# Kernel tuning notes

Measured on AMD Instinct MI355X. Metric: run time of the kernel, lower is better.

## Reference

```python
import jax, jax.numpy as jnp
import numpy as np

HID = 128
N_LAYERS = 4


def setup_inputs() -> dict:
    key = jax.random.key(0)
    ks = jax.random.split(key, 16)
    B, T, N, F = 64, 168, 64, 17
    x = jax.random.normal(ks[0], (B, T, N, F), dtype=jnp.float32)
    adj = jax.random.randint(ks[1], (N, N), 0, 2, dtype=jnp.int32)
    s = 0.05
    W1 = jax.random.normal(ks[2], (F, HID), dtype=jnp.float32) * s
    a1 = jax.random.normal(ks[3], (2 * HID,), dtype=jnp.float32) * s
    W2 = jax.random.normal(ks[4], (HID, HID), dtype=jnp.float32) * s
    a2 = jax.random.normal(ks[5], (2 * HID,), dtype=jnp.float32) * s
    # PyTorch LSTM weights, 4 layers, gate order i,f,g,o; layer0 input=HID
    Wih = jax.random.normal(ks[6], (N_LAYERS, 4 * HID, HID), dtype=jnp.float32) * s
    Whh = jax.random.normal(ks[7], (N_LAYERS, 4 * HID, HID), dtype=jnp.float32) * s
    bih = jax.random.normal(ks[8], (N_LAYERS, 4 * HID), dtype=jnp.float32) * s
    bhh = jax.random.normal(ks[9], (N_LAYERS, 4 * HID), dtype=jnp.float32) * s
    Wlin = jax.random.normal(ks[10], (1, N_LAYERS * HID), dtype=jnp.float32) * s
    blin = jax.random.normal(ks[11], (1,), dtype=jnp.float32) * s
    return {"x": x, "adj": adj, "W1": W1, "a1": a1, "W2": W2, "a2": a2,
            "Wih": Wih, "Whh": Whh, "bih": bih, "bhh": bhh,
            "Wlin": Wlin, "blin": blin, "site_idx": 10}


def _gat(x, W, a, adj_mask):
    # x: [B,T,N,F] -> h: [B,T,N,O]; dense adjacency-masked attention
    h = jnp.einsum('btnf,fo->btno', x, W)
    O = W.shape[1]
    src = h @ a[:O]          # [B,T,N]  a^T[Wh_i || .]
    dst = h @ a[O:]          # [B,T,N]  a^T[. || Wh_j]
    e = jax.nn.leaky_relu(src[..., :, None] + dst[..., None, :], 0.2)  # [B,T,N,N]
    e = jnp.where(adj_mask, e, jnp.float32(-1e9))
    attn = jax.nn.softmax(e, axis=-1)
    return jnp.einsum('btij,btjo->btio', attn, h)


def _lstm_layer(x_seq, Wih_l, Whh_l, b_l):
    # x_seq: [B,T,H]; PyTorch gate order i,f,g,o
    B = x_seq.shape[0]
    h0 = jnp.zeros((B, HID), x_seq.dtype)

    def step(carry, x_t):
        h, c = carry
        g = x_t @ Wih_l.T + h @ Whh_l.T + b_l
        i, f, gg, o = jnp.split(g, 4, axis=-1)
        c = jax.nn.sigmoid(f) * c + jax.nn.sigmoid(i) * jnp.tanh(gg)
        h = jax.nn.sigmoid(o) * jnp.tanh(c)
        return (h, c), h

    (hT, cT), ys = jax.lax.scan(step, (h0, h0), jnp.swapaxes(x_seq, 0, 1))
    return jnp.swapaxes(ys, 0, 1), hT


def reference(x, adj, W1, a1, W2, a2, Wih, Whh, bih, bhh, Wlin, blin, site_idx):
    N = adj.shape[0]
    adj_mask = (adj > 0) | jnp.eye(N, dtype=bool)  # self-loops avoid empty rows
    h = _gat(x, W1, a1, adj_mask)
    h = _gat(h, W2, a2, adj_mask)
    seq = h[:, :, site_idx, :]                     # [B,T,HID]
    h_finals = []
    for l in range(N_LAYERS):
        seq, hT = _lstm_layer(seq, Wih[l], Whh[l], bih[l] + bhh[l])
        h_finals.append(hT)
    hcat = jnp.concatenate(h_finals, axis=-1)      # [B, 4*HID] == permute+reshape
    out = hcat @ Wlin.T + blin                     # [B,1]
    return out.squeeze(-1)
```

## Files before the change

### kernel.cpp

```cpp
#include <hip/hip_runtime.h>
#include <hip/hip_bf16.h>

#define BB 64
#define TT 168
#define NN 64
#define FF 17
#define HID 128
#define GATES 512
#define NLAYERS 4
#define NROWS (BB*TT)

#define CH 8
#define NCHUNK (TT/CH)

#define WS_W1SRC 0
#define WS_W1DST 32
#define WS_W2SRC 64
#define WS_W2DST 192
#define WS_BSUM  320
#define WS_WD    2560
#define WS_WSV   2592
#define WS_W12   2624
#define WS_WXG0T 4800
#define WS_ADJB  15104
#define WS_FLAGS 16000
#define WS_XG    1395712
#define WS_HSEQ0 6900736
#define HSEQ_SZ  1376256

__device__ __forceinline__ void lds_barrier() {
    __asm__ volatile("" ::: "memory");
    __builtin_amdgcn_s_waitcnt(0xc07f);
    __builtin_amdgcn_s_barrier();
    __asm__ volatile("" ::: "memory");
}

__device__ __forceinline__ float fsig(float x) {
    return __builtin_amdgcn_rcpf(1.f + __expf(-x));
}
__device__ __forceinline__ float ftanh(float x) {
    float e = __expf(2.f * x);
    return 1.f - 2.f * __builtin_amdgcn_rcpf(e + 1.f);
}
__device__ __forceinline__ float bcast_lane(float v, int lane) {
    return __int_as_float(__builtin_amdgcn_readlane(__float_as_int(v), lane));
}

__global__ void prep1(const float* __restrict__ W1, const float* __restrict__ a1,
                      const float* __restrict__ W2, const float* __restrict__ a2,
                      const float* __restrict__ bih, const float* __restrict__ bhh,
                      const int* __restrict__ adj, float* __restrict__ ws) {
    int tid = threadIdx.x;
    if (tid < 34) {
        int f = tid % FF, half = tid / FF;
        float acc = 0.f;
        for (int o = 0; o < HID; o++) acc += W1[f*HID + o] * a1[half*HID + o];
        ws[(half ? WS_W1DST : WS_W1SRC) + f] = acc;
    }
    {
        int k = tid & 127, half = tid >> 7;
        float acc = 0.f;
        for (int o = 0; o < HID; o++) acc += W2[k*HID + o] * a2[half*HID + o];
        ws[(half ? WS_W2DST : WS_W2SRC) + k] = acc;
    }
    for (int idx = tid; idx < NLAYERS*GATES; idx += 256) ws[WS_BSUM + idx] = bih[idx] + bhh[idx];
    if (tid < 64) {
        unsigned long long m = 1ull << tid;
        const int* ar = adj + tid*64;
        for (int j = 0; j < 64; j++) if (ar[j] > 0) m |= (1ull << j);
        ((unsigned long long*)(ws + WS_ADJB))[tid] = m;
    }
    __hip_atomic_store((int*)(ws + WS_FLAGS) + tid, 0,
                       __ATOMIC_RELAXED, __HIP_MEMORY_SCOPE_AGENT);
}

__global__ void prep2(const float* __restrict__ W1, const float* __restrict__ W2,
                      float* __restrict__ ws) {
    int f = blockIdx.x, o = threadIdx.x;
    float acc = 0.f;
    for (int k = 0; k < HID; k++) acc += W1[f*HID + k] * W2[k*HID + o];
    ws[WS_W12 + f*HID + o] = acc;
}

__global__ void prep3(const float* __restrict__ W1, const float* __restrict__ Wih0,
                      float* __restrict__ ws) {
    int idx = blockIdx.x * 256 + threadIdx.x;
    if (idx < 17) {
        int f = idx;
        float acc = 0.f;
        for (int k = 0; k < HID; k++) acc += W1[f*HID + k] * ws[WS_W2DST + k];
        ws[WS_WD + f] = acc;
    } else if (idx < 34) {
        int f = idx - 17;
        float acc = 0.f;
        for (int k = 0; k < HID; k++) acc += W1[f*HID + k] * ws[WS_W2SRC + k];
        ws[WS_WSV + f] = acc;
    } else if (idx < 34 + GATES*FF) {
        int e = idx - 34;
        int j = e % GATES, f = e / GATES;
        float acc = 0.f;
        for (int o = 0; o < HID; o++) acc += ws[WS_W12 + f*HID + o] * Wih0[j*HID + o];
        ws[WS_WXG0T + j*20 + f] = acc;
    }
}

struct __align__(16) GatSmem {
    float attn[64*68];
    float xsT[FF*64];
    float xbarT[FF*68];
    float src1[64], dst1[64], rinv[64], att2[64];
    float xbar2[20];
    float part_x[FF*8];
    unsigned long long adjbits[64];
};

__global__ __launch_bounds__(256) void gat_fused(const float* __restrict__ x, const int* __restrict__ adj,
                                                 const float* __restrict__ ws,
                                                 float* __restrict__ Xg, const int* __restrict__ site_ptr) {
    __shared__ GatSmem sm;
    const int tid = threadIdx.x;
    const int tt = blockIdx.x, bb = blockIdx.y;
    const int site = site_ptr[0];
    const int r = bb*TT + tt;
    const float* xblk = x + (size_t)r * (NN*FF);

    for (int idx = tid; idx < NN*FF; idx += 256) {
        int n = idx / FF, f = idx % FF;
        sm.xsT[f*64 + n] = xblk[idx];
    }
    if (tid < 64) sm.adjbits[tid] = ((const unsigned long long*)(ws + WS_ADJB))[tid];
    lds_barrier();

    if (tid < 128) {
        int n = tid & 63, half = tid >> 6;
        const float* wv = ws + (half ? WS_W1DST : WS_W1SRC);
        float acc = 0.f;
        #pragma unroll
        for (int f = 0; f < FF; f++) acc += sm.xsT[f*64 + n] * wv[f];
        if (half) sm.dst1[n] = acc; else sm.src1[n] = acc;
    }
    lds_barrier();

    {
        int q = tid & 3, i = tid >> 2;
        unsigned long long ab = sm.adjbits[i];
        float si = sm.src1[i];
        float v[16];
        float vmax = -1e30f;
        #pragma unroll
        for (int u = 0; u < 16; u++) {
            int jj = q*16 + u;
            float e = si + sm.dst1[jj];
            float lv = fmaxf(e, 0.2f*e);
            lv = ((ab >> jj) & 1ull) ? lv : -1e9f;
            v[u] = lv;
            vmax = fmaxf(vmax, lv);
        }
        vmax = fmaxf(vmax, __shfl_xor(vmax, 1, 4));
        vmax = fmaxf(vmax, __shfl_xor(vmax, 2, 4));
        float s = 0.f;
        float* arow = &sm.attn[i*68];
        #pragma unroll
        for (int w = 0; w < 4; w++) {
            float4 pv;
            pv.x = __expf(v[w*4+0] - vmax);
            pv.y = __expf(v[w*4+1] - vmax);
            pv.z = __expf(v[w*4+2] - vmax);
            pv.w = __expf(v[w*4+3] - vmax);
            s += (pv.x + pv.y) + (pv.z + pv.w);
            *(float4*)(arow + q*16 + w*4) = pv;
        }
        s += __shfl_xor(s, 1, 4);
        s += __shfl_xor(s, 2, 4);
        if (q == 0) sm.rinv[i] = 1.f / s;
    }
    lds_barrier();

    {
        int i = tid & 63, q = tid >> 6;
        const float* arow = &sm.attn[i*68];
        float acc[5] = {0.f,0.f,0.f,0.f,0.f};
        const int nf = (q == 0) ? 5 : 4;
        for (int j4 = 0; j4 < 16; j4++) {
            float4 a4 = *(const float4*)(arow + j4*4);
            #pragma unroll
            for (int u = 0; u < 5; u++) {
                if (u < nf) {
                    int f = q + 4*u;
                    float4 x4 = *(const float4*)(&sm.xsT[f*64 + j4*4]);
                    acc[u] += a4.x*x4.x + a4.y*x4.y + a4.z*x4.z + a4.w*x4.w;
                }
            }
        }
        float ri = sm.rinv[i];
        #pragma unroll
        for (int u = 0; u < 5; u++) {
            if (u < nf) sm.xbarT[(q + 4*u)*68 + i] = acc[u] * ri;
        }
    }
    lds_barrier();

    if (tid < 64) {
        int jj = tid;
        float d = 0.f, sp = 0.f;
        #pragma unroll
        for (int f = 0; f < FF; f++) {
            float xv = sm.xbarT[f*68 + jj];
            float xs = sm.xbarT[f*68 + site];
            d  += xv * ws[WS_WD + f];
            sp += xs * ws[WS_WSV + f];
        }
        unsigned long long ab = sm.adjbits[site];
        float e = sp + d;
        float lv = fmaxf(e, 0.2f*e);
        lv = ((ab >> jj) & 1ull) ? lv : -1e9f;
        float m = lv;
        #pragma unroll
        for (int dd = 1; dd < 64; dd <<= 1) m = fmaxf(m, __shfl_xor(m, dd));
        float p = __expf(lv - m);
        float s = p;
        #pragma unroll
        for (int dd = 1; dd < 64; dd <<= 1) s += __shfl_xor(s, dd);
        sm.att2[jj] = p / s;
    }
    lds_barrier();

    if (tid < FF*8) {
        int f = tid >> 3, c = tid & 7;
        float p = 0.f;
        #pragma unroll
        for (int u = 0; u < 8; u++) {
            int i = c*8 + u;
            p += sm.att2[i] * sm.xbarT[f*68 + i];
        }
        sm.part_x[f*8 + c] = p;
    }
    lds_barrier();

    if (tid < FF) {
        float s = 0.f;
        #pragma unroll
        for (int c = 0; c < 8; c++) s += sm.part_x[tid*8 + c];
        sm.xbar2[tid] = s;
    }
    lds_barrier();

    {
        float xb[FF];
        #pragma unroll
        for (int f = 0; f < FF; f++) xb[f] = sm.xbar2[f];
        #pragma unroll
        for (int half = 0; half < 2; half++) {
            int j = tid + half*256;
            const float4* wp = (const float4*)(ws + WS_WXG0T + j*20);
            float4 w0 = wp[0], w1 = wp[1], w2 = wp[2], w3 = wp[3];
            float wlast = ws[WS_WXG0T + j*20 + 16];
            float acc = ws[WS_BSUM + j];
            acc += w0.x*xb[0] + w0.y*xb[1] + w0.z*xb[2] + w0.w*xb[3];
            acc += w1.x*xb[4] + w1.y*xb[5] + w1.z*xb[6] + w1.w*xb[7];
            acc += w2.x*xb[8] + w2.y*xb[9] + w2.z*xb[10] + w2.w*xb[11];
            acc += w3.x*xb[12] + w3.y*xb[13] + w3.z*xb[14] + w3.w*xb[15];
            acc += wlast*xb[16];
            Xg[(size_t)r*GATES + j] = acc;
        }
    }
}

__global__ __launch_bounds__(512, 1) void lstm_pipe(const float* __restrict__ Xg0,
                                                    const float* __restrict__ Wih,
                                                    const float* __restrict__ Whh,
                                                    float* __restrict__ ws) {
    const int b = blockIdx.x;
    const int l = blockIdx.y;
    const int tid = threadIdx.x;
    const int lane = tid & 63;
    const int kc = tid >> 7;
    const int jj = tid & 127;
    const int o = kc*32 + (lane & 31);
    const bool blane = (lane < 32);
    const bool storer = ((tid >> 6) & 1) == 0;

    __shared__ __align__(16) float part[2][4][128][4];
    __shared__ __align__(16) float xg[2][CH*GATES];
    __shared__ __align__(16) float xs[2][CH*HID];

    int* flags = (int*)(ws + WS_FLAGS);

    float w[4][32];
    {
        const float* Whh_l = Whh + (size_t)l*GATES*HID;
        #pragma unroll
        for (int u = 0; u < 4; u++) {
            const float4* wr2 = (const float4*)(Whh_l + (size_t)(u*128 + jj)*HID + kc*32);
            #pragma unroll
            for (int k4 = 0; k4 < 8; k4++) {
                float4 v = wr2[k4];
                w[u][k4*4+0] = v.x; w[u][k4*4+1] = v.y; w[u][k4*4+2] = v.z; w[u][k4*4+3] = v.w;
            }
        }
    }

    const float* xg_g  = Xg0 + (size_t)b*TT*GATES;
    float*       hout  = ws + WS_HSEQ0 + (size_t)l*HSEQ_SZ + (size_t)b*TT*HID;
    const float* hprev = (l > 0) ? (ws + WS_HSEQ0 + (size_t)(l-1)*HSEQ_SZ + (size_t)b*TT*HID)
                                 : ws;
    const float* Wih_l = Wih + (size_t)l*GATES*HID;
    const float  bsum_j = ws[WS_BSUM + l*GATES + tid];
    const float4* wr = (const float4*)(Wih_l + (size_t)tid*HID);

    float h_own = 0.f, c_own = 0.f;
    float4 pf0 = {0,0,0,0}, pf1 = {0,0,0,0};
    int buf = 0;

    float acc[CH];
    float4 wv0, wv1, wv2, wv3;

    if (l == 0) {
        const float4* g4 = (const float4*)xg_g;
        float4 v0 = g4[tid], v1 = g4[512 + tid];
        float4* d = (float4*)xg[0];
        d[tid] = v0; d[512 + tid] = v1;
        lds_barrier();
    } else {
        if (tid == 0) {
            int* flg = &flags[(l-1)*BB + b];
            while (__hip_atomic_load(flg, __ATOMIC_RELAXED, __HIP_MEMORY_SCOPE_AGENT) < CH)
                __builtin_amdgcn_s_sleep(8);
        }
        lds_barrier();
        #pragma unroll
        for (int q = 0; q < 2; q++) {
            int idx = q*512 + tid;
            xs[0][idx] = __hip_atomic_load(&hprev[idx],
                                           __ATOMIC_RELAXED, __HIP_MEMORY_SCOPE_AGENT);
        }
        lds_barrier();
        float a0[CH];
        #pragma unroll
        for (int t = 0; t < CH; t++) a0[t] = bsum_j;
        #pragma unroll
        for (int kq = 0; kq < 4; kq++) {
            float4 wvv[8];
            #pragma unroll
            for (int q = 0; q < 8; q++) wvv[q] = wr[kq*8 + q];
            #pragma unroll
            for (int t = 0; t < CH; t++) {
                const float4* xp = (const float4*)(&xs[0][t*HID + kq*32]);
                float a = 0.f;
                #pragma unroll
                for (int q = 0; q < 8; q++) {
                    float4 xv = xp[q];
                    a += wvv[q].x*xv.x + wvv[q].y*xv.y + wvv[q].z*xv.z + wvv[q].w*xv.w;
                }
                a0[t] += a;
            }
        }
        #pragma unroll
        for (int t = 0; t < CH; t++) xg[0][t*GATES + tid] = a0[t];
        wv0 = wr[0]; wv1 = wr[1]; wv2 = wr[2]; wv3 = wr[3];
        #pragma unroll
        for (int t = 0; t < CH; t++) acc[t] = bsum_j;
        lds_barrier();
    }

    for (int c = 0; c < NCHUNK; c++) {
        const bool have_next = (c + 1 < NCHUNK);

        if (l == 0) {
            if (have_next) {
                const float4* g4 = (const float4*)(xg_g + (size_t)(c+1)*CH*GATES);
                pf0 = g4[tid]; pf1 = g4[512 + tid];
            }
        } else if (have_next) {
            if (tid == 0) {
                int* flg = &flags[(l-1)*BB + b];
                const int need = (c + 2)*CH;
                while (__hip_atomic_load(flg, __ATOMIC_RELAXED, __HIP_MEMORY_SCOPE_AGENT) < need)
                    __builtin_amdgcn_s_sleep(8);
            }
            lds_barrier();
            float v0 = __hip_atomic_load(&hprev[(size_t)(c+1)*CH*HID + tid],
                                         __ATOMIC_RELAXED, __HIP_MEMORY_SCOPE_AGENT);
            float v1 = __hip_atomic_load(&hprev[(size_t)(c+1)*CH*HID + 512 + tid],
                                         __ATOMIC_RELAXED, __HIP_MEMORY_SCOPE_AGENT);
            xs[(c+1)&1][tid] = v0;
            xs[(c+1)&1][512 + tid] = v1;
        }

        const float* xgbuf = (l == 0) ? xg[buf] : xg[c & 1];
        const float* xsn = xs[(c+1)&1];
        float* xgn = xg[(c+1)&1];

        for (int tc = 0; tc < CH; tc++) {
            const int t = c*CH + tc;
            float xgc[4];
            if (blane) {
                #pragma unroll
                for (int u = 0; u < 4; u++) xgc[u] = xgbuf[tc*GATES + u*HID + o];
            }
            float a0 = 0.f, a1 = 0.f, a2 = 0.f, a3 = 0.f;
            #pragma unroll
            for (int k = 0; k < 32; k++) {
                float hv = bcast_lane(h_own, k);
                a0 += w[0][k]*hv; a1 += w[1][k]*hv; a2 += w[2][k]*hv; a3 += w[3][k]*hv;
            }
            float4 st = {a0, a1, a2, a3};
            *(float4*)(&part[t & 1][kc][jj][0]) = st;

            lds_barrier();

            if (l > 0 && have_next) {
                const int kb = tc*16;
                #pragma unroll
                for (int t2 = 0; t2 < CH; t2++) {
                    const float4* xp = (const float4*)(&xsn[t2*HID + kb]);
                    float4 x0 = xp[0], x1 = xp[1], x2 = xp[2], x3 = xp[3];
                    acc[t2] += wv0.x*x0.x + wv0.y*x0.y + wv0.z*x0.z + wv0.w*x0.w
                             + wv1.x*x1.x + wv1.y*x1.y + wv1.z*x1.z + wv1.w*x1.w
                             + wv2.x*x2.x + wv2.y*x2.y + wv2.z*x2.z + wv2.w*x2.w
                             + wv3.x*x3.x + wv3.y*x3.y + wv3.z*x3.z + wv3.w*x3.w;
                }
                const int ns = (tc + 1) & 7;
                wv0 = wr[ns*4+0]; wv1 = wr[ns*4+1]; wv2 = wr[ns*4+2]; wv3 = wr[ns*4+3];
                if (tc == CH-1) {
                    #pragma unroll
                    for (int t2 = 0; t2 < CH; t2++) {
                        xgn[t2*GATES + tid] = acc[t2];
                        acc[t2] = bsum_j;
                    }
                }
            }

            if (blane) {
                float4 s4 = {xgc[0], xgc[1], xgc[2], xgc[3]};
                #pragma unroll
                for (int kcc = 0; kcc < 4; kcc++) {
                    float4 p = *(const float4*)(&part[t & 1][kcc][o][0]);
                    s4.x += p.x; s4.y += p.y; s4.z += p.z; s4.w += p.w;
                }
                float si = fsig(s4.x), sf = fsig(s4.y), so = fsig(s4.w);
                float tg = ftanh(s4.z);
                c_own = sf*c_own + si*tg;
                h_own = so*ftanh(c_own);
                if (storer)
                    __hip_atomic_store(&hout[t*HID + o], h_own,
                                       __ATOMIC_RELAXED, __HIP_MEMORY_SCOPE_AGENT);
            }
        }

        if (l == 0) {
            __asm__ volatile("s_waitcnt vmcnt(0)" ::: "memory");
            if (have_next) {
                float4* d = (float4*)xg[buf ^ 1];
                d[tid] = pf0; d[512 + tid] = pf1;
                buf ^= 1;
            }
            lds_barrier();
            if (tid == 0)
                __hip_atomic_store(&flags[b], (c+1)*CH,
                                   __ATOMIC_RELAXED, __HIP_MEMORY_SCOPE_AGENT);
        } else {
            __asm__ volatile("s_waitcnt vmcnt(0)" ::: "memory");
            lds_barrier();
            if (l < NLAYERS - 1 && tid == 0)
                __hip_atomic_store(&flags[l*BB + b], (c+1)*CH,
                                   __ATOMIC_RELAXED, __HIP_MEMORY_SCOPE_AGENT);
        }
    }
}

__global__ void final_lin(const float* __restrict__ ws, const float* __restrict__ Wlin,
                          const float* __restrict__ blin, float* __restrict__ out) {
    const int b = blockIdx.x, l = threadIdx.x;
    float acc = 0.f;
    #pragma unroll
    for (int u = 0; u < 8; u++) {
        int idx = u*64 + l;
        int layer = idx >> 7, k = idx & 127;
        const float* hs = ws + WS_HSEQ0 + (size_t)layer*HSEQ_SZ;
        acc += hs[((size_t)b*TT + (TT-1))*HID + k] * Wlin[idx];
    }
    #pragma unroll
    for (int d = 1; d < 64; d <<= 1) acc += __shfl_xor(acc, d);
    if (l == 0) out[b] = acc + blin[0];
}

extern "C" void kernel_launch(void* const* d_in, const int* in_sizes, int n_in,
                              void* d_out, int out_size, void* d_ws, size_t ws_size,
                              hipStream_t stream) {
    const float* x    = (const float*)d_in[0];
    const int*   adj  = (const int*)d_in[1];
    const float* W1   = (const float*)d_in[2];
    const float* a1   = (const float*)d_in[3];
    const float* W2   = (const float*)d_in[4];
    const float* a2   = (const float*)d_in[5];
    const float* Wih  = (const float*)d_in[6];
    const float* Whh  = (const float*)d_in[7];
    const float* bih  = (const float*)d_in[8];
    const float* bhh  = (const float*)d_in[9];
    const float* Wlin = (const float*)d_in[10];
    const float* blin = (const float*)d_in[11];
    const int*   site = (const int*)d_in[12];
    float* ws  = (float*)d_ws;
    float* out = (float*)d_out;

    prep1<<<1, 256, 0, stream>>>(W1, a1, W2, a2, bih, bhh, adj, ws);
    prep2<<<FF, 128, 0, stream>>>(W1, W2, ws);
    prep3<<<35, 256, 0, stream>>>(W1, Wih, ws);
    gat_fused<<<dim3(TT, BB), 256, 0, stream>>>(x, adj, ws, ws + WS_XG, site);
    lstm_pipe<<<dim3(BB, NLAYERS), 512, 0, stream>>>(ws + WS_XG, Wih, Whh, ws);
    final_lin<<<64, 64, 0, stream>>>(ws, Wlin, blin, out);
}
```

Baseline: 586.7 us.

## Keep previous-layer hidden chunk in registers and broadcast via readlane for input projection

The lower layer's hidden chunk is now staged through a small padded LDS tile and loaded once into 16 registers per lane. The input-gate projection for the next chunk then uses readlane broadcasts instead of repeated LDS float4 reads. That projection is also moved after the gate nonlinearity, so it overlaps with the recurrent critical path rather than sitting between the barrier and the cell update. Flag handoffs switch from relaxed to acquire/release ordering, and inline-asm pins force the recurrent weights and broadcast values to stay in VGPRs. The cost is more register pressure and many readlane (scalar) operations, plus extra barriers per chunk.

```diff
diff --git a/kernel.cpp b/kernel.cpp
--- a/kernel.cpp
+++ b/kernel.cpp
@@ -27,6 +27,8 @@
 #define WS_XG    1395712
 #define WS_HSEQ0 6900736
 #define HSEQ_SZ  1376256
+
+#define PIN(x) __asm__ volatile("" : "+v"(x))
 
 __device__ __forceinline__ void lds_barrier() {
     __asm__ volatile("" ::: "memory");
@@ -282,7 +284,7 @@
 
     __shared__ __align__(16) float part[2][4][128][4];
     __shared__ __align__(16) float xg[2][CH*GATES];
-    __shared__ __align__(16) float xs[2][CH*HID];
+    __shared__ __align__(16) float xsl[64*17];
 
     int* flags = (int*)(ws + WS_FLAGS);
 
@@ -294,9 +296,14 @@
             const float4* wr2 = (const float4*)(Whh_l + (size_t)(u*128 + jj)*HID + kc*32);
             #pragma unroll
             for (int k4 = 0; k4 < 8; k4++) {
-                float4 v = wr2[k4];
-                w[u][k4*4+0] = v.x; w[u][k4*4+1] = v.y; w[u][k4*4+2] = v.z; w[u][k4*4+3] = v.w;
-            }
+                float4 v4 = wr2[k4];
+                w[u][k4*4+0] = v4.x; w[u][k4*4+1] = v4.y; w[u][k4*4+2] = v4.z; w[u][k4*4+3] = v4.w;
+            }
+        }
+        #pragma unroll
+        for (int u = 0; u < 4; u++) {
+            #pragma unroll
+            for (int k = 0; k < 32; k++) PIN(w[u][k]);
         }
     }
 
@@ -313,6 +320,7 @@
     int buf = 0;
 
     float acc[CH];
+    float v[16];
     float4 wv0, wv1, wv2, wv3;
 
     if (l == 0) {
@@ -324,35 +332,39 @@
     } else {
         if (tid == 0) {
             int* flg = &flags[(l-1)*BB + b];
-            while (__hip_atomic_load(flg, __ATOMIC_RELAXED, __HIP_MEMORY_SCOPE_AGENT) < CH)
+            while (__hip_atomic_load(flg, __ATOMIC_ACQUIRE, __HIP_MEMORY_SCOPE_AGENT) < CH)
                 __builtin_amdgcn_s_sleep(8);
         }
         lds_barrier();
-        #pragma unroll
-        for (int q = 0; q < 2; q++) {
-            int idx = q*512 + tid;
-            xs[0][idx] = __hip_atomic_load(&hprev[idx],
-                                           __ATOMIC_RELAXED, __HIP_MEMORY_SCOPE_AGENT);
+        {
+            float s0 = __hip_atomic_load(&hprev[tid],       __ATOMIC_RELAXED, __HIP_MEMORY_SCOPE_AGENT);
+            float s1 = __hip_atomic_load(&hprev[512 + tid], __ATOMIC_RELAXED, __HIP_MEMORY_SCOPE_AGENT);
+            int i0 = tid, i1 = 512 + tid;
+            xsl[(i0 >> 4)*17 + (i0 & 15)] = s0;
+            xsl[(i1 >> 4)*17 + (i1 & 15)] = s1;
         }
         lds_barrier();
+        #pragma unroll
+        for (int m = 0; m < 16; m++) { v[m] = xsl[lane*17 + m]; PIN(v[m]); }
+
         float a0[CH];
         #pragma unroll
         for (int t = 0; t < CH; t++) a0[t] = bsum_j;
-        #pragma unroll
-        for (int kq = 0; kq < 4; kq++) {
-            float4 wvv[8];
+        for (int s = 0; s < CH; s++) {
+            float4 q0 = wr[s*4+0], q1 = wr[s*4+1], q2 = wr[s*4+2], q3 = wr[s*4+3];
             #pragma unroll
-            for (int q = 0; q < 8; q++) wvv[q] = wr[kq*8 + q];
-            #pragma unroll
-            for (int t = 0; t < CH; t++) {
-                const float4* xp = (const float4*)(&xs[0][t*HID + kq*32]);
-                float a = 0.f;
-                #pragma unroll
-                for (int q = 0; q < 8; q++) {
-                    float4 xv = xp[q];
-                    a += wvv[q].x*xv.x + wvv[q].y*xv.y + wvv[q].z*xv.z + wvv[q].w*xv.w;
-                }
-                a0[t] += a;
+            for (int t2 = 0; t2 < CH; t2++) {
+                const int src = t2*8 + s;
+                float a = a0[t2];
+                a += q0.x*bcast_lane(v[0],  src); a += q0.y*bcast_lane(v[1],  src);
+                a += q0.z*bcast_lane(v[2],  src); a += q0.w*bcast_lane(v[3],  src);
+                a += q1.x*bcast_lane(v[4],  src); a += q1.y*bcast_lane(v[5],  src);
+                a += q1.z*bcast_lane(v[6],  src); a += q1.w*bcast_lane(v[7],  src);
+                a += q2.x*bcast_lane(v[8],  src); a += q2.y*bcast_lane(v[9],  src);
+                a += q2.z*bcast_lane(v[10], src); a += q2.w*bcast_lane(v[11], src);
+                a += q3.x*bcast_lane(v[12], src); a += q3.y*bcast_lane(v[13], src);
+                a += q3.z*bcast_lane(v[14], src); a += q3.w*bcast_lane(v[15], src);
+                a0[t2] = a;
             }
         }
         #pragma unroll
@@ -375,21 +387,26 @@
             if (tid == 0) {
                 int* flg = &flags[(l-1)*BB + b];
                 const int need = (c + 2)*CH;
-                while (__hip_atomic_load(flg, __ATOMIC_RELAXED, __HIP_MEMORY_SCOPE_AGENT) < need)
+                while (__hip_atomic_load(flg, __ATOMIC_ACQUIRE, __HIP_MEMORY_SCOPE_AGENT) < need)
                     __builtin_amdgcn_s_sleep(8);
             }
             lds_barrier();
-            float v0 = __hip_atomic_load(&hprev[(size_t)(c+1)*CH*HID + tid],
-                                         __ATOMIC_RELAXED, __HIP_MEMORY_SCOPE_AGENT);
-            float v1 = __hip_atomic_load(&hprev[(size_t)(c+1)*CH*HID + 512 + tid],
-                                         __ATOMIC_RELAXED, __HIP_MEMORY_SCOPE_AGENT);
-            xs[(c+1)&1][tid] = v0;
-            xs[(c+1)&1][512 + tid] = v1;
+            {
+                float s0 = __hip_atomic_load(&hprev[(size_t)(c+1)*CH*HID + tid],
+                                             __ATOMIC_RELAXED, __HIP_MEMORY_SCOPE_AGENT);
+                float s1 = __hip_atomic_load(&hprev[(size_t)(c+1)*CH*HID + 512 + tid],
+                                             __ATOMIC_RELAXED, __HIP_MEMORY_SCOPE_AGENT);
+                int i0 = tid, i1 = 512 + tid;
+                xsl[(i0 >> 4)*17 + (i0 & 15)] = s0;
+                xsl[(i1 >> 4)*17 + (i1 & 15)] = s1;
+            }
+            lds_barrier();
+            #pragma unroll
+            for (int m = 0; m < 16; m++) { v[m] = xsl[lane*17 + m]; PIN(v[m]); }
         }
 
         const float* xgbuf = (l == 0) ? xg[buf] : xg[c & 1];
-        const float* xsn = xs[(c+1)&1];
-        float* xgn = xg[(c+1)&1];
+        float* xgn = xg[(c+1) & 1];
 
         for (int tc = 0; tc < CH; tc++) {
             const int t = c*CH + tc;
@@ -408,28 +425,6 @@
             *(float4*)(&part[t & 1][kc][jj][0]) = st;
 
             lds_barrier();
-
-            if (l > 0 && have_next) {
-                const int kb = tc*16;
-                #pragma unroll
-                for (int t2 = 0; t2 < CH; t2++) {
-                    const float4* xp = (const float4*)(&xsn[t2*HID + kb]);
-                    float4 x0 = xp[0], x1 = xp[1], x2 = xp[2], x3 = xp[3];
-                    acc[t2] += wv0.x*x0.x + wv0.y*x0.y + wv0.z*x0.z + wv0.w*x0.w
-                             + wv1.x*x1.x + wv1.y*x1.y + wv1.z*x1.z + wv1.w*x1.w
-                             + wv2.x*x2.x + wv2.y*x2.y + wv2.z*x2.z + wv2.w*x2.w
-                             + wv3.x*x3.x + wv3.y*x3.y + wv3.z*x3.z + wv3.w*x3.w;
-                }
-                const int ns = (tc + 1) & 7;
-                wv0 = wr[ns*4+0]; wv1 = wr[ns*4+1]; wv2 = wr[ns*4+2]; wv3 = wr[ns*4+3];
-                if (tc == CH-1) {
-                    #pragma unroll
-                    for (int t2 = 0; t2 < CH; t2++) {
-                        xgn[t2*GATES + tid] = acc[t2];
-                        acc[t2] = bsum_j;
-                    }
-                }
-            }
 
             if (blane) {
                 float4 s4 = {xgc[0], xgc[1], xgc[2], xgc[3]};
@@ -446,6 +441,32 @@
                     __hip_atomic_store(&hout[t*HID + o], h_own,
                                        __ATOMIC_RELAXED, __HIP_MEMORY_SCOPE_AGENT);
             }
+
+            if (l > 0 && have_next) {
+                #pragma unroll
+                for (int t2 = 0; t2 < CH; t2++) {
+                    const int src = t2*8 + tc;
+                    float a = acc[t2];
+                    a += wv0.x*bcast_lane(v[0],  src); a += wv0.y*bcast_lane(v[1],  src);
+                    a += wv0.z*bcast_lane(v[2],  src); a += wv0.w*bcast_lane(v[3],  src);
+                    a += wv1.x*bcast_lane(v[4],  src); a += wv1.y*bcast_lane(v[5],  src);
+                    a += wv1.z*bcast_lane(v[6],  src); a += wv1.w*bcast_lane(v[7],  src);
+                    a += wv2.x*bcast_lane(v[8],  src); a += wv2.y*bcast_lane(v[9],  src);
+                    a += wv2.z*bcast_lane(v[10], src); a += wv2.w*bcast_lane(v[11], src);
+                    a += wv3.x*bcast_lane(v[12], src); a += wv3.y*bcast_lane(v[13], src);
+                    a += wv3.z*bcast_lane(v[14], src); a += wv3.w*bcast_lane(v[15], src);
+                    acc[t2] = a;
+                }
+                const int ns = (tc + 1) & 7;
+                wv0 = wr[ns*4+0]; wv1 = wr[ns*4+1]; wv2 = wr[ns*4+2]; wv3 = wr[ns*4+3];
+                if (tc == CH-1) {
+                    #pragma unroll
+                    for (int t2 = 0; t2 < CH; t2++) {
+                        xgn[t2*GATES + tid] = acc[t2];
+                        acc[t2] = bsum_j;
+                    }
+                }
+            }
         }
 
         if (l == 0) {
@@ -458,13 +479,13 @@
             lds_barrier();
             if (tid == 0)
                 __hip_atomic_store(&flags[b], (c+1)*CH,
-                                   __ATOMIC_RELAXED, __HIP_MEMORY_SCOPE_AGENT);
+                                   __ATOMIC_RELEASE, __HIP_MEMORY_SCOPE_AGENT);
         } else {
             __asm__ volatile("s_waitcnt vmcnt(0)" ::: "memory");
             lds_barrier();
             if (l < NLAYERS - 1 && tid == 0)
                 __hip_atomic_store(&flags[l*BB + b], (c+1)*CH,
-                                   __ATOMIC_RELAXED, __HIP_MEMORY_SCOPE_AGENT);
+                                   __ATOMIC_RELEASE, __HIP_MEMORY_SCOPE_AGENT);
         }
     }
 }
```

Measured after the change: 738.7 us. 25.9% more time.

## Process two batch rows per LSTM pipeline block to share weight registers

Applied to the files above, without the earlier changes.

Each lstm_pipe block now handles two batch rows, so the grid drops from 64x4 to 32x4 blocks and the register-resident Whh slice and the Wih stream are reused across both rows. The gate epilogue is moved ahead of the input-projection work, and the per-group flags and LDS buffers are indexed per row. This halves the number of blocks and doubles the per-step work on the serial recurrence path. It trades parallelism (fewer CUs busy) for reuse, and doubles LDS usage.

```diff
diff --git a/kernel.cpp b/kernel.cpp
--- a/kernel.cpp
+++ b/kernel.cpp
@@ -12,6 +12,8 @@
 
 #define CH 8
 #define NCHUNK (TT/CH)
+#define NB 2
+#define NG (BB/NB)
 
 #define WS_W1SRC 0
 #define WS_W1DST 32
@@ -270,7 +272,7 @@
                                                     const float* __restrict__ Wih,
                                                     const float* __restrict__ Whh,
                                                     float* __restrict__ ws) {
-    const int b = blockIdx.x;
+    const int g = blockIdx.x;
     const int l = blockIdx.y;
     const int tid = threadIdx.x;
     const int lane = tid & 63;
@@ -280,9 +282,9 @@
     const bool blane = (lane < 32);
     const bool storer = ((tid >> 6) & 1) == 0;
 
-    __shared__ __align__(16) float part[2][4][128][4];
-    __shared__ __align__(16) float xg[2][CH*GATES];
-    __shared__ __align__(16) float xs[2][CH*HID];
+    __shared__ __align__(16) float part[2][4][NB][128][4];
+    __shared__ __align__(16) float xg[2][NB][CH*GATES];
+    __shared__ __align__(16) float xs[2][NB][CH*HID];
 
     int* flags = (int*)(ws + WS_FLAGS);
 
@@ -294,72 +296,82 @@
             const float4* wr2 = (const float4*)(Whh_l + (size_t)(u*128 + jj)*HID + kc*32);
             #pragma unroll
             for (int k4 = 0; k4 < 8; k4++) {
-                float4 v = wr2[k4];
-                w[u][k4*4+0] = v.x; w[u][k4*4+1] = v.y; w[u][k4*4+2] = v.z; w[u][k4*4+3] = v.w;
-            }
-        }
-    }
-
-    const float* xg_g  = Xg0 + (size_t)b*TT*GATES;
-    float*       hout  = ws + WS_HSEQ0 + (size_t)l*HSEQ_SZ + (size_t)b*TT*HID;
-    const float* hprev = (l > 0) ? (ws + WS_HSEQ0 + (size_t)(l-1)*HSEQ_SZ + (size_t)b*TT*HID)
-                                 : ws;
-    const float* Wih_l = Wih + (size_t)l*GATES*HID;
-    const float  bsum_j = ws[WS_BSUM + l*GATES + tid];
-    const float4* wr = (const float4*)(Wih_l + (size_t)tid*HID);
-
-    float h_own = 0.f, c_own = 0.f;
-    float4 pf0 = {0,0,0,0}, pf1 = {0,0,0,0};
+                float4 v4 = wr2[k4];
+                w[u][k4*4+0] = v4.x; w[u][k4*4+1] = v4.y; w[u][k4*4+2] = v4.z; w[u][k4*4+3] = v4.w;
+            }
+        }
+    }
+
+    const float* xgg[NB];
+    float*       houtb[NB];
+    const float* hprevb[NB];
+    #pragma unroll
+    for (int bb = 0; bb < NB; bb++) {
+        xgg[bb]    = Xg0 + (size_t)(g*NB + bb)*TT*GATES;
+        houtb[bb]  = ws + WS_HSEQ0 + (size_t)l*HSEQ_SZ + (size_t)(g*NB + bb)*TT*HID;
+        hprevb[bb] = (l > 0) ? (ws + WS_HSEQ0 + (size_t)(l-1)*HSEQ_SZ + (size_t)(g*NB + bb)*TT*HID)
+                             : ws;
+    }
+    const float  bs = ws[WS_BSUM + l*GATES + tid];
+    const float4* wr = (const float4*)(Wih + (size_t)l*GATES*HID + (size_t)tid*HID);
+
+    float h_own[NB] = {0.f, 0.f}, c_own[NB] = {0.f, 0.f};
+    float4 pf[NB][2];
     int buf = 0;
-
-    float acc[CH];
+    float acc[NB][CH];
     float4 wv0, wv1, wv2, wv3;
 
     if (l == 0) {
-        const float4* g4 = (const float4*)xg_g;
-        float4 v0 = g4[tid], v1 = g4[512 + tid];
-        float4* d = (float4*)xg[0];
-        d[tid] = v0; d[512 + tid] = v1;
+        #pragma unroll
+        for (int bb = 0; bb < NB; bb++) {
+            const float4* g4 = (const float4*)xgg[bb];
+            float4* d = (float4*)xg[0][bb];
+            d[tid] = g4[tid]; d[512 + tid] = g4[512 + tid];
+        }
         lds_barrier();
     } else {
         if (tid == 0) {
-            int* flg = &flags[(l-1)*BB + b];
+            int* flg = &flags[(l-1)*NG + g];
             while (__hip_atomic_load(flg, __ATOMIC_RELAXED, __HIP_MEMORY_SCOPE_AGENT) < CH)
                 __builtin_amdgcn_s_sleep(8);
         }
         lds_barrier();
         #pragma unroll
-        for (int q = 0; q < 2; q++) {
-            int idx = q*512 + tid;
-            xs[0][idx] = __hip_atomic_load(&hprev[idx],
-                                           __ATOMIC_RELAXED, __HIP_MEMORY_SCOPE_AGENT);
-        }
+        for (int bb = 0; bb < NB; bb++)
+            #pragma unroll
+            for (int q = 0; q < 2; q++) {
+                int idx = q*512 + tid;
+                xs[0][bb][idx] = __hip_atomic_load(&hprevb[bb][idx],
+                                                   __ATOMIC_RELAXED, __HIP_MEMORY_SCOPE_AGENT);
+            }
         lds_barrier();
-        float a0[CH];
-        #pragma unroll
-        for (int t = 0; t < CH; t++) a0[t] = bsum_j;
-        #pragma unroll
-        for (int kq = 0; kq < 4; kq++) {
-            float4 wvv[8];
-            #pragma unroll
-            for (int q = 0; q < 8; q++) wvv[q] = wr[kq*8 + q];
-            #pragma unroll
-            for (int t = 0; t < CH; t++) {
-                const float4* xp = (const float4*)(&xs[0][t*HID + kq*32]);
-                float a = 0.f;
-                #pragma unroll
-                for (int q = 0; q < 8; q++) {
-                    float4 xv = xp[q];
-                    a += wvv[q].x*xv.x + wvv[q].y*xv.y + wvv[q].z*xv.z + wvv[q].w*xv.w;
-                }
-                a0[t] += a;
-            }
-        }
-        #pragma unroll
-        for (int t = 0; t < CH; t++) xg[0][t*GATES + tid] = a0[t];
+        #pragma unroll
+        for (int bb = 0; bb < NB; bb++)
+            #pragma unroll
+            for (int t = 0; t < CH; t++) acc[bb][t] = bs;
+        for (int s = 0; s < CH; s++) {
+            float4 q0 = wr[s*4+0], q1 = wr[s*4+1], q2 = wr[s*4+2], q3 = wr[s*4+3];
+            #pragma unroll
+            for (int bb = 0; bb < NB; bb++)
+                #pragma unroll
+                for (int t2 = 0; t2 < CH; t2++) {
+                    const float4* xp = (const float4*)(&xs[0][bb][t2*HID + s*16]);
+                    float4 x0 = xp[0], x1 = xp[1], x2 = xp[2], x3 = xp[3];
+                    acc[bb][t2] += q0.x*x0.x + q0.y*x0.y + q0.z*x0.z + q0.w*x0.w
+                                 + q1.x*x1.x + q1.y*x1.y + q1.z*x1.z + q1.w*x1.w
+                                 + q2.x*x2.x + q2.y*x2.y + q2.z*x2.z + q2.w*x2.w
+                                 + q3.x*x3.x + q3.y*x3.y + q3.z*x3.z + q3.w*x3.w;
+                }
+        }
+        #pragma unroll
+        for (int bb = 0; bb < NB; bb++)
+            #pragma unroll
+            for (int t = 0; t < CH; t++) xg[0][bb][t*GATES + tid] = acc[bb][t];
         wv0 = wr[0]; wv1 = wr[1]; wv2 = wr[2]; wv3 = wr[3];
         #pragma unroll
-        for (int t = 0; t < CH; t++) acc[t] = bsum_j;
+        for (int bb = 0; bb < NB; bb++)
+            #pragma unroll
+            for (int t = 0; t < CH; t++) acc[bb][t] = bs;
         lds_barrier();
     }
 
@@ -368,102 +380,132 @@
 
         if (l == 0) {
             if (have_next) {
-                const float4* g4 = (const float4*)(xg_g + (size_t)(c+1)*CH*GATES);
-                pf0 = g4[tid]; pf1 = g4[512 + tid];
+                #pragma unroll
+                for (int bb = 0; bb < NB; bb++) {
+                    const float4* g4 = (const float4*)(xgg[bb] + (size_t)(c+1)*CH*GATES);
+                    pf[bb][0] = g4[tid]; pf[bb][1] = g4[512 + tid];
+                }
             }
         } else if (have_next) {
             if (tid == 0) {
-                int* flg = &flags[(l-1)*BB + b];
+                int* flg = &flags[(l-1)*NG + g];
                 const int need = (c + 2)*CH;
                 while (__hip_atomic_load(flg, __ATOMIC_RELAXED, __HIP_MEMORY_SCOPE_AGENT) < need)
                     __builtin_amdgcn_s_sleep(8);
             }
             lds_barrier();
-            float v0 = __hip_atomic_load(&hprev[(size_t)(c+1)*CH*HID + tid],
-                                         __ATOMIC_RELAXED, __HIP_MEMORY_SCOPE_AGENT);
-            float v1 = __hip_atomic_load(&hprev[(size_t)(c+1)*CH*HID + 512 + tid],
-                                         __ATOMIC_RELAXED, __HIP_MEMORY_SCOPE_AGENT);
-            xs[(c+1)&1][tid] = v0;
-            xs[(c+1)&1][512 + tid] = v1;
-        }
-
-        const float* xgbuf = (l == 0) ? xg[buf] : xg[c & 1];
-        const float* xsn = xs[(c+1)&1];
-        float* xgn = xg[(c+1)&1];
+            #pragma unroll
+            for (int bb = 0; bb < NB; bb++)
+                #pragma unroll
+                for (int q = 0; q < 2; q++) {
+                    int idx = q*512 + tid;
+                    xs[(c+1)&1][bb][idx] = __hip_atomic_load(&hprevb[bb][(size_t)(c+1)*CH*HID + idx],
+                                                             __ATOMIC_RELAXED, __HIP_MEMORY_SCOPE_AGENT);
+                }
+        }
+
+        const int cb  = (l == 0) ? buf : (c & 1);
+        const int nb_ = (c + 1) & 1;
 
         for (int tc = 0; tc < CH; tc++) {
             const int t = c*CH + tc;
-            float xgc[4];
+            float xgc[NB][4];
             if (blane) {
                 #pragma unroll
-                for (int u = 0; u < 4; u++) xgc[u] = xgbuf[tc*GATES + u*HID + o];
-            }
-            float a0 = 0.f, a1 = 0.f, a2 = 0.f, a3 = 0.f;
+                for (int bb = 0; bb < NB; bb++)
+                    #pragma unroll
+                    for (int u = 0; u < 4; u++)
+                        xgc[bb][u] = xg[cb][bb][tc*GATES + u*HID + o];
+            }
+            float aa[NB][4];
+            #pragma unroll
+            for (int bb = 0; bb < NB; bb++) {
+                aa[bb][0] = 0.f; aa[bb][1] = 0.f; aa[bb][2] = 0.f; aa[bb][3] = 0.f;
+            }
             #pragma unroll
             for (int k = 0; k < 32; k++) {
-                float hv = bcast_lane(h_own, k);
-                a0 += w[0][k]*hv; a1 += w[1][k]*hv; a2 += w[2][k]*hv; a3 += w[3][k]*hv;
-            }
-            float4 st = {a0, a1, a2, a3};
-            *(float4*)(&part[t & 1][kc][jj][0]) = st;
+                float hv0 = bcast_lane(h_own[0], k);
+                float hv1 = bcast_lane(h_own[1], k);
+                aa[0][0] += w[0][k]*hv0; aa[0][1] += w[1][k]*hv0;
+                aa[0][2] += w[2][k]*hv0; aa[0][3] += w[3][k]*hv0;
+                aa[1][0] += w[0][k]*hv1; aa[1][1] += w[1][k]*hv1;
+                aa[1][2] += w[2][k]*hv1; aa[1][3] += w[3][k]*hv1;
+            }
+            #pragma unroll
+            for (int bb = 0; bb < NB; bb++) {
+                float4 st = {aa[bb][0], aa[bb][1], aa[bb][2], aa[bb][3]};
+                *(float4*)(&part[t & 1][kc][bb][jj][0]) = st;
+            }
 
             lds_barrier();
+
+            if (blane) {
+                #pragma unroll
+                for (int bb = 0; bb < NB; bb++) {
+                    float4 p0 = *(const float4*)(&part[t & 1][0][bb][o][0]);
+                    float4 p1 = *(const float4*)(&part[t & 1][1][bb][o][0]);
+                    float4 p2 = *(const float4*)(&part[t & 1][2][bb][o][0]);
+                    float4 p3 = *(const float4*)(&part[t & 1][3][bb][o][0]);
+                    float gi = xgc[bb][0] + ((p0.x + p1.x) + (p2.x + p3.x));
+                    float gf = xgc[bb][1] + ((p0.y + p1.y) + (p2.y + p3.y));
+                    float gg = xgc[bb][2] + ((p0.z + p1.z) + (p2.z + p3.z));
+                    float go = xgc[bb][3] + ((p0.w + p1.w) + (p2.w + p3.w));
+                    float si = fsig(gi), sf = fsig(gf), so = fsig(go);
+                    float tg = ftanh(gg);
+                    c_own[bb] = sf*c_own[bb] + si*tg;
+                    h_own[bb] = so*ftanh(c_own[bb]);
+                    if (storer)
+                        __hip_atomic_store(&houtb[bb][t*HID + o], h_own[bb],
+                                           __ATOMIC_RELAXED, __HIP_MEMORY_SCOPE_AGENT);
+                }
+            }
 
             if (l > 0 && have_next) {
                 const int kb = tc*16;
                 #pragma unroll
-                for (int t2 = 0; t2 < CH; t2++) {
-                    const float4* xp = (const float4*)(&xsn[t2*HID + kb]);
-                    float4 x0 = xp[0], x1 = xp[1], x2 = xp[2], x3 = xp[3];
-                    acc[t2] += wv0.x*x0.x + wv0.y*x0.y + wv0.z*x0.z + wv0.w*x0.w
-                             + wv1.x*x1.x + wv1.y*x1.y + wv1.z*x1.z + wv1.w*x1.w
-                             + wv2.x*x2.x + wv2.y*x2.y + wv2.z*x2.z + wv2.w*x2.w
-                             + wv3.x*x3.x + wv3.y*x3.y + wv3.z*x3.z + wv3.w*x3.w;
-                }
+                for (int bb = 0; bb < NB; bb++)
+                    #pragma unroll
+                    for (int t2 = 0; t2 < CH; t2++) {
+                        const float4* xp = (const float4*)(&xs[nb_][bb][t2*HID + kb]);
+                        float4 x0 = xp[0], x1 = xp[1], x2 = xp[2], x3 = xp[3];
+                        acc[bb][t2] += wv0.x*x0.x + wv0.y*x0.y + wv0.z*x0.z + wv0.w*x0.w
+                                     + wv1.x*x1.x + wv1.y*x1.y + wv1.z*x1.z + wv1.w*x1.w
+                                     + wv2.x*x2.x + wv2.y*x2.y + wv2.z*x2.z + wv2.w*x2.w
+                                     + wv3.x*x3.x + wv3.y*x3.y + wv3.z*x3.z + wv3.w*x3.w;
+                    }
                 const int ns = (tc + 1) & 7;
                 wv0 = wr[ns*4+0]; wv1 = wr[ns*4+1]; wv2 = wr[ns*4+2]; wv3 = wr[ns*4+3];
-                if (tc == CH-1) {
+                if (tc == CH - 1) {
                     #pragma unroll
-                    for (int t2 = 0; t2 < CH; t2++) {
-                        xgn[t2*GATES + tid] = acc[t2];
-                        acc[t2] = bsum_j;
-                    }
-                }
-            }
-
-            if (blane) {
-                float4 s4 = {xgc[0], xgc[1], xgc[2], xgc[3]};
-                #pragma unroll
-                for (int kcc = 0; kcc < 4; kcc++) {
-                    float4 p = *(const float4*)(&part[t & 1][kcc][o][0]);
-                    s4.x += p.x; s4.y += p.y; s4.z += p.z; s4.w += p.w;
-                }
-                float si = fsig(s4.x), sf = fsig(s4.y), so = fsig(s4.w);
-                float tg = ftanh(s4.z);
-                c_own = sf*c_own + si*tg;
-                h_own = so*ftanh(c_own);
-                if (storer)
-                    __hip_atomic_store(&hout[t*HID + o], h_own,
-                                       __ATOMIC_RELAXED, __HIP_MEMORY_SCOPE_AGENT);
+                    for (int bb = 0; bb < NB; bb++)
+                        #pragma unroll
+                        for (int t2 = 0; t2 < CH; t2++) {
+                            xg[nb_][bb][t2*GATES + tid] = acc[bb][t2];
+                            acc[bb][t2] = bs;
+                        }
+                }
             }
         }
 
         if (l == 0) {
             __asm__ volatile("s_waitcnt vmcnt(0)" ::: "memory");
             if (have_next) {
-                float4* d = (float4*)xg[buf ^ 1];
-                d[tid] = pf0; d[512 + tid] = pf1;
+                #pragma unroll
+                for (int bb = 0; bb < NB; bb++) {
+                    float4* d = (float4*)xg[buf ^ 1][bb];
+                    d[tid] = pf[bb][0]; d[512 + tid] = pf[bb][1];
+                }
                 buf ^= 1;
             }
             lds_barrier();
             if (tid == 0)
-                __hip_atomic_store(&flags[b], (c+1)*CH,
+                __hip_atomic_store(&flags[g], (c+1)*CH,
                                    __ATOMIC_RELAXED, __HIP_MEMORY_SCOPE_AGENT);
         } else {
             __asm__ volatile("s_waitcnt vmcnt(0)" ::: "memory");
             lds_barrier();
             if (l < NLAYERS - 1 && tid == 0)
-                __hip_atomic_store(&flags[l*BB + b], (c+1)*CH,
+                __hip_atomic_store(&flags[l*NG + g], (c+1)*CH,
                                    __ATOMIC_RELAXED, __HIP_MEMORY_SCOPE_AGENT);
         }
     }
@@ -508,6 +550,6 @@
     prep2<<<FF, 128, 0, stream>>>(W1, W2, ws);
     prep3<<<35, 256, 0, stream>>>(W1, Wih, ws);
     gat_fused<<<dim3(TT, BB), 256, 0, stream>>>(x, adj, ws, ws + WS_XG, site);
-    lstm_pipe<<<dim3(BB, NLAYERS), 512, 0, stream>>>(ws + WS_XG, Wih, Whh, ws);
+    lstm_pipe<<<dim3(NG, NLAYERS), 512, 0, stream>>>(ws + WS_XG, Wih, Whh, ws);
     final_lin<<<64, 64, 0, stream>>>(ws, Wlin, blin, out);
 }
```

New measurement: 930.3 us. 58.6% more time.

## Double LSTM block to 1024 threads, splitting recurrent K into 8 slices

Applied to the files above, without the earlier changes.

Each LSTM block now runs 1024 threads instead of 512. The recurrent h·Whh product is split into 8 K-slices of 16 instead of 4 of 32, which cuts the serial per-step broadcast/FMA chain and the register-held weights per thread. The next-chunk input projection is redistributed so each thread computes 4 timesteps for one gate row, and it now runs after the gate update instead of before it. The cost is more partial sums to reduce through LDS each step and a larger block whose barriers must synchronize 16 waves.

```diff
diff --git a/kernel.cpp b/kernel.cpp
--- a/kernel.cpp
+++ b/kernel.cpp
@@ -206,9 +206,9 @@
         #pragma unroll
         for (int f = 0; f < FF; f++) {
             float xv = sm.xbarT[f*68 + jj];
-            float xs = sm.xbarT[f*68 + site];
+            float xsv = sm.xbarT[f*68 + site];
             d  += xv * ws[WS_WD + f];
-            sp += xs * ws[WS_WSV + f];
+            sp += xsv * ws[WS_WSV + f];
         }
         unsigned long long ab = sm.adjbits[site];
         float e = sp + d;
@@ -266,37 +266,36 @@
     }
 }
 
-__global__ __launch_bounds__(512, 1) void lstm_pipe(const float* __restrict__ Xg0,
-                                                    const float* __restrict__ Wih,
-                                                    const float* __restrict__ Whh,
-                                                    float* __restrict__ ws) {
+__global__ __launch_bounds__(1024) void lstm_pipe(const float* __restrict__ Xg0,
+                                                  const float* __restrict__ Wih,
+                                                  const float* __restrict__ Whh,
+                                                  float* __restrict__ ws) {
     const int b = blockIdx.x;
     const int l = blockIdx.y;
     const int tid = threadIdx.x;
     const int lane = tid & 63;
+    const int w_ = tid >> 6;
     const int kc = tid >> 7;
     const int jj = tid & 127;
-    const int o = kc*32 + (lane & 31);
-    const bool blane = (lane < 32);
-    const bool storer = ((tid >> 6) & 1) == 0;
-
-    __shared__ __align__(16) float part[2][4][128][4];
+    const int o = kc*16 + (lane & 15);
+    const bool storer = ((w_ & 1) == 0) && (lane < 16);
+    const int jg = (kc & 3)*128 + jj;
+    const int tbase = (kc >> 2)*4;
+
+    __shared__ __align__(16) float part[2][8][128][4];
     __shared__ __align__(16) float xg[2][CH*GATES];
     __shared__ __align__(16) float xs[2][CH*HID];
 
     int* flags = (int*)(ws + WS_FLAGS);
 
-    float w[4][32];
+    float4 w4[4][4];
     {
         const float* Whh_l = Whh + (size_t)l*GATES*HID;
         #pragma unroll
-        for (int u = 0; u < 4; u++) {
-            const float4* wr2 = (const float4*)(Whh_l + (size_t)(u*128 + jj)*HID + kc*32);
+        for (int g = 0; g < 4; g++) {
+            const float4* p = (const float4*)(Whh_l + (size_t)(g*128 + jj)*HID + kc*16);
             #pragma unroll
-            for (int k4 = 0; k4 < 8; k4++) {
-                float4 v = wr2[k4];
-                w[u][k4*4+0] = v.x; w[u][k4*4+1] = v.y; w[u][k4*4+2] = v.z; w[u][k4*4+3] = v.w;
-            }
+            for (int q = 0; q < 4; q++) w4[g][q] = p[q];
         }
     }
 
@@ -304,22 +303,16 @@
     float*       hout  = ws + WS_HSEQ0 + (size_t)l*HSEQ_SZ + (size_t)b*TT*HID;
     const float* hprev = (l > 0) ? (ws + WS_HSEQ0 + (size_t)(l-1)*HSEQ_SZ + (size_t)b*TT*HID)
                                  : ws;
-    const float* Wih_l = Wih + (size_t)l*GATES*HID;
-    const float  bsum_j = ws[WS_BSUM + l*GATES + tid];
-    const float4* wr = (const float4*)(Wih_l + (size_t)tid*HID);
+    const float4* wrg = (const float4*)(Wih + (size_t)l*GATES*HID + (size_t)jg*HID);
+    const float  bsg = ws[WS_BSUM + l*GATES + jg];
 
     float h_own = 0.f, c_own = 0.f;
-    float4 pf0 = {0,0,0,0}, pf1 = {0,0,0,0};
+    float4 pf = {0,0,0,0};
     int buf = 0;
-
-    float acc[CH];
-    float4 wv0, wv1, wv2, wv3;
+    float acc[4];
 
     if (l == 0) {
-        const float4* g4 = (const float4*)xg_g;
-        float4 v0 = g4[tid], v1 = g4[512 + tid];
-        float4* d = (float4*)xg[0];
-        d[tid] = v0; d[512 + tid] = v1;
+        ((float4*)xg[0])[tid] = ((const float4*)xg_g)[tid];
         lds_barrier();
     } else {
         if (tid == 0) {
@@ -328,38 +321,28 @@
                 __builtin_amdgcn_s_sleep(8);
         }
         lds_barrier();
-        #pragma unroll
-        for (int q = 0; q < 2; q++) {
-            int idx = q*512 + tid;
-            xs[0][idx] = __hip_atomic_load(&hprev[idx],
-                                           __ATOMIC_RELAXED, __HIP_MEMORY_SCOPE_AGENT);
-        }
+        xs[0][tid] = __hip_atomic_load(&hprev[tid], __ATOMIC_RELAXED, __HIP_MEMORY_SCOPE_AGENT);
         lds_barrier();
-        float a0[CH];
-        #pragma unroll
-        for (int t = 0; t < CH; t++) a0[t] = bsum_j;
-        #pragma unroll
-        for (int kq = 0; kq < 4; kq++) {
-            float4 wvv[8];
+        float a[4];
+        #pragma unroll
+        for (int u = 0; u < 4; u++) a[u] = bsg;
+        for (int s = 0; s < CH; s++) {
+            float4 q0 = wrg[s*4+0], q1 = wrg[s*4+1], q2 = wrg[s*4+2], q3 = wrg[s*4+3];
             #pragma unroll
-            for (int q = 0; q < 8; q++) wvv[q] = wr[kq*8 + q];
-            #pragma unroll
-            for (int t = 0; t < CH; t++) {
-                const float4* xp = (const float4*)(&xs[0][t*HID + kq*32]);
-                float a = 0.f;
-                #pragma unroll
-                for (int q = 0; q < 8; q++) {
-                    float4 xv = xp[q];
-                    a += wvv[q].x*xv.x + wvv[q].y*xv.y + wvv[q].z*xv.z + wvv[q].w*xv.w;
-                }
-                a0[t] += a;
-            }
-        }
-        #pragma unroll
-        for (int t = 0; t < CH; t++) xg[0][t*GATES + tid] = a0[t];
-        wv0 = wr[0]; wv1 = wr[1]; wv2 = wr[2]; wv3 = wr[3];
-        #pragma unroll
-        for (int t = 0; t < CH; t++) acc[t] = bsum_j;
+            for (int u = 0; u < 4; u++) {
+                const float4* xp = (const float4*)(&xs[0][(tbase+u)*HID + s*16]);
+                float4 x0 = xp[0], x1 = xp[1], x2 = xp[2], x3 = xp[3];
+                a[u] += q0.x*x0.x + q0.y*x0.y + q0.z*x0.z + q0.w*x0.w
+                      + q1.x*x1.x + q1.y*x1.y + q1.z*x1.z + q1.w*x1.w
+                      + q2.x*x2.x + q2.y*x2.y + q2.z*x2.z + q2.w*x2.w
+                      + q3.x*x3.x + q3.y*x3.y + q3.z*x3.z + q3.w*x3.w;
+            }
+        }
+        #pragma unroll
+        for (int u = 0; u < 4; u++) {
+            xg[0][(tbase+u)*GATES + jg] = a[u];
+            acc[u] = bsg;
+        }
         lds_barrier();
     }
 
@@ -367,10 +350,7 @@
         const bool have_next = (c + 1 < NCHUNK);
 
         if (l == 0) {
-            if (have_next) {
-                const float4* g4 = (const float4*)(xg_g + (size_t)(c+1)*CH*GATES);
-                pf0 = g4[tid]; pf1 = g4[512 + tid];
-            }
+            if (have_next) pf = ((const float4*)(xg_g + (size_t)(c+1)*CH*GATES))[tid];
         } else if (have_next) {
             if (tid == 0) {
                 int* flg = &flags[(l-1)*BB + b];
@@ -379,80 +359,84 @@
                     __builtin_amdgcn_s_sleep(8);
             }
             lds_barrier();
-            float v0 = __hip_atomic_load(&hprev[(size_t)(c+1)*CH*HID + tid],
-                                         __ATOMIC_RELAXED, __HIP_MEMORY_SCOPE_AGENT);
-            float v1 = __hip_atomic_load(&hprev[(size_t)(c+1)*CH*HID + 512 + tid],
-                                         __ATOMIC_RELAXED, __HIP_MEMORY_SCOPE_AGENT);
-            xs[(c+1)&1][tid] = v0;
-            xs[(c+1)&1][512 + tid] = v1;
+            xs[(c+1)&1][tid] = __hip_atomic_load(&hprev[(size_t)(c+1)*CH*HID + tid],
+                                                 __ATOMIC_RELAXED, __HIP_MEMORY_SCOPE_AGENT);
         }
 
         const float* xgbuf = (l == 0) ? xg[buf] : xg[c & 1];
-        const float* xsn = xs[(c+1)&1];
-        float* xgn = xg[(c+1)&1];
+        const int nb_ = (c + 1) & 1;
 
         for (int tc = 0; tc < CH; tc++) {
             const int t = c*CH + tc;
-            float xgc[4];
-            if (blane) {
-                #pragma unroll
-                for (int u = 0; u < 4; u++) xgc[u] = xgbuf[tc*GATES + u*HID + o];
-            }
+            float xgc0 = xgbuf[tc*GATES + 0*HID + o];
+            float xgc1 = xgbuf[tc*GATES + 1*HID + o];
+            float xgc2 = xgbuf[tc*GATES + 2*HID + o];
+            float xgc3 = xgbuf[tc*GATES + 3*HID + o];
+
             float a0 = 0.f, a1 = 0.f, a2 = 0.f, a3 = 0.f;
             #pragma unroll
-            for (int k = 0; k < 32; k++) {
-                float hv = bcast_lane(h_own, k);
-                a0 += w[0][k]*hv; a1 += w[1][k]*hv; a2 += w[2][k]*hv; a3 += w[3][k]*hv;
+            for (int q = 0; q < 4; q++) {
+                float h0 = bcast_lane(h_own, q*4+0);
+                float h1 = bcast_lane(h_own, q*4+1);
+                float h2 = bcast_lane(h_own, q*4+2);
+                float h3 = bcast_lane(h_own, q*4+3);
+                a0 += w4[0][q].x*h0 + w4[0][q].y*h1 + w4[0][q].z*h2 + w4[0][q].w*h3;
+                a1 += w4[1][q].x*h0 + w4[1][q].y*h1 + w4[1][q].z*h2 + w4[1][q].w*h3;
+                a2 += w4[2][q].x*h0 + w4[2][q].y*h1 + w4[2][q].z*h2 + w4[2][q].w*h3;
+                a3 += w4[3][q].x*h0 + w4[3][q].y*h1 + w4[3][q].z*h2 + w4[3][q].w*h3;
             }
             float4 st = {a0, a1, a2, a3};
             *(float4*)(&part[t & 1][kc][jj][0]) = st;
 
             lds_barrier();
 
-            if (l > 0 && have_next) {
-                const int kb = tc*16;
-                #pragma unroll
-                for (int t2 = 0; t2 < CH; t2++) {
-                    const float4* xp = (const float4*)(&xsn[t2*HID + kb]);
-                    float4 x0 = xp[0], x1 = xp[1], x2 = xp[2], x3 = xp[3];
-                    acc[t2] += wv0.x*x0.x + wv0.y*x0.y + wv0.z*x0.z + wv0.w*x0.w
-                             + wv1.x*x1.x + wv1.y*x1.y + wv1.z*x1.z + wv1.w*x1.w
-                             + wv2.x*x2.x + wv2.y*x2.y + wv2.z*x2.z + wv2.w*x2.w
-                             + wv3.x*x3.x + wv3.y*x3.y + wv3.z*x3.z + wv3.w*x3.w;
-                }
-                const int ns = (tc + 1) & 7;
-                wv0 = wr[ns*4+0]; wv1 = wr[ns*4+1]; wv2 = wr[ns*4+2]; wv3 = wr[ns*4+3];
-                if (tc == CH-1) {
-                    #pragma unroll
-                    for (int t2 = 0; t2 < CH; t2++) {
-                        xgn[t2*GATES + tid] = acc[t2];
-                        acc[t2] = bsum_j;
-                    }
-                }
-            }
-
-            if (blane) {
-                float4 s4 = {xgc[0], xgc[1], xgc[2], xgc[3]};
-                #pragma unroll
-                for (int kcc = 0; kcc < 4; kcc++) {
-                    float4 p = *(const float4*)(&part[t & 1][kcc][o][0]);
-                    s4.x += p.x; s4.y += p.y; s4.z += p.z; s4.w += p.w;
-                }
-                float si = fsig(s4.x), sf = fsig(s4.y), so = fsig(s4.w);
-                float tg = ftanh(s4.z);
+            {
+                float4 p0 = *(const float4*)(&part[t & 1][0][o][0]);
+                float4 p1 = *(const float4*)(&part[t & 1][1][o][0]);
+                float4 p2 = *(const float4*)(&part[t & 1][2][o][0]);
+                float4 p3 = *(const float4*)(&part[t & 1][3][o][0]);
+                float4 p4 = *(const float4*)(&part[t & 1][4][o][0]);
+                float4 p5 = *(const float4*)(&part[t & 1][5][o][0]);
+                float4 p6 = *(const float4*)(&part[t & 1][6][o][0]);
+                float4 p7 = *(const float4*)(&part[t & 1][7][o][0]);
+                float gi = xgc0 + (((p0.x+p1.x)+(p2.x+p3.x)) + ((p4.x+p5.x)+(p6.x+p7.x)));
+                float gf = xgc1 + (((p0.y+p1.y)+(p2.y+p3.y)) + ((p4.y+p5.y)+(p6.y+p7.y)));
+                float gg = xgc2 + (((p0.z+p1.z)+(p2.z+p3.z)) + ((p4.z+p5.z)+(p6.z+p7.z)));
+                float go = xgc3 + (((p0.w+p1.w)+(p2.w+p3.w)) + ((p4.w+p5.w)+(p6.w+p7.w)));
+                float si = fsig(gi), sf = fsig(gf), so = fsig(go);
+                float tg = ftanh(gg);
                 c_own = sf*c_own + si*tg;
                 h_own = so*ftanh(c_own);
                 if (storer)
                     __hip_atomic_store(&hout[t*HID + o], h_own,
                                        __ATOMIC_RELAXED, __HIP_MEMORY_SCOPE_AGENT);
             }
+
+            if (l > 0 && have_next) {
+                float4 wv0 = wrg[tc*4+0], wv1 = wrg[tc*4+1], wv2 = wrg[tc*4+2], wv3 = wrg[tc*4+3];
+                #pragma unroll
+                for (int u = 0; u < 4; u++) {
+                    const float4* xp = (const float4*)(&xs[nb_][(tbase+u)*HID + tc*16]);
+                    float4 x0 = xp[0], x1 = xp[1], x2 = xp[2], x3 = xp[3];
+                    acc[u] += wv0.x*x0.x + wv0.y*x0.y + wv0.z*x0.z + wv0.w*x0.w
+                            + wv1.x*x1.x + wv1.y*x1.y + wv1.z*x1.z + wv1.w*x1.w
+                            + wv2.x*x2.x + wv2.y*x2.y + wv2.z*x2.z + wv2.w*x2.w
+                            + wv3.x*x3.x + wv3.y*x3.y + wv3.z*x3.z + wv3.w*x3.w;
+                }
+                if (tc == CH - 1) {
+                    #pragma unroll
+                    for (int u = 0; u < 4; u++) {
+                        xg[nb_][(tbase+u)*GATES + jg] = acc[u];
+                        acc[u] = bsg;
+                    }
+                }
+            }
         }
 
         if (l == 0) {
             __asm__ volatile("s_waitcnt vmcnt(0)" ::: "memory");
             if (have_next) {
-                float4* d = (float4*)xg[buf ^ 1];
-                d[tid] = pf0; d[512 + tid] = pf1;
+                ((float4*)xg[buf ^ 1])[tid] = pf;
                 buf ^= 1;
             }
             lds_barrier();
@@ -508,6 +492,6 @@
     prep2<<<FF, 128, 0, stream>>>(W1, W2, ws);
     prep3<<<35, 256, 0, stream>>>(W1, Wih, ws);
     gat_fused<<<dim3(TT, BB), 256, 0, stream>>>(x, adj, ws, ws + WS_XG, site);
-    lstm_pipe<<<dim3(BB, NLAYERS), 512, 0, stream>>>(ws + WS_XG, Wih, Whh, ws);
+    lstm_pipe<<<dim3(BB, NLAYERS), 1024, 0, stream>>>(ws + WS_XG, Wih, Whh, ws);
     final_lin<<<64, 64, 0, stream>>>(ws, Wlin, blin, out);
 }
```

Result: slower. 1.311 ms (+123.5%).
